# Kernel tuning notes

Hardware: AMD Instinct MI355X
Metric: run time of the kernel (lower is better)

Reference implementation:

```python
import jax, jax.numpy as jnp
import numpy as np

NUM_EXPERTS = 8
TOP_K = 2
AUX_COEF = 0.01
B, S, D, H = 4, 2048, 1024, 684


def setup_inputs() -> dict:
    key = jax.random.key(0)
    ks = jax.random.split(key, 5)
    scale_d = 1.0 / np.sqrt(D)
    scale_h = 1.0 / np.sqrt(H)
    return {
        "x": jax.random.normal(ks[0], (B, S, D), dtype=jnp.float32),
        "router_w": jax.random.normal(ks[1], (NUM_EXPERTS, D), dtype=jnp.float32) * scale_d,
        "w1": jax.random.normal(ks[2], (NUM_EXPERTS, H, D), dtype=jnp.float32) * scale_d,
        "w2": jax.random.normal(ks[3], (NUM_EXPERTS, D, H), dtype=jnp.float32) * scale_h,
        "w3": jax.random.normal(ks[4], (NUM_EXPERTS, H, D), dtype=jnp.float32) * scale_d,
    }


def reference(x, router_w, w1, w2, w3):
    b, s, d = x.shape
    xf = x.reshape(-1, d)                                   # [T, d]
    probs = jax.nn.softmax(xf @ router_w.T, axis=-1)        # [T, E]
    topk_probs, topk_idx = jax.lax.top_k(probs, TOP_K)      # [T, k]

    # aux load-balancing loss (uses top-1 assignment density)
    density = jnp.mean(jax.nn.one_hot(topk_idx[:, 0], NUM_EXPERTS, dtype=xf.dtype), axis=0)
    aux_loss = AUX_COEF * jnp.sum(density * probs.mean(axis=0)) * NUM_EXPERTS

    # per-token per-expert combine weight (sums probs if an expert repeats across slots)
    combine = jnp.sum(jax.nn.one_hot(topk_idx, NUM_EXPERTS, dtype=xf.dtype)
                      * topk_probs[..., None], axis=1)      # [T, E]

    out = jnp.zeros_like(xf)
    for e in range(NUM_EXPERTS):  # fixed small expert loop
        h = jax.nn.silu(xf @ w1[e].T) * (xf @ w3[e].T)      # [T, H] SwiGLU
        out = out + combine[:, e:e + 1] * (h @ w2[e].T)     # weighted scatter-combine
    return out.reshape(b, s, d), aux_loss
```

## Files before the change

kernel.cpp:

```cpp
#include <hip/hip_runtime.h>
#include <hip/hip_bf16.h>

#define T_TOK 8192
#define DMODEL 1024
#define HDIM 684
#define HPAD 704
#define NEXP 8

typedef short  bf16x8  __attribute__((ext_vector_type(8)));
typedef float  f32x4   __attribute__((ext_vector_type(4)));

__device__ inline unsigned short f2bu(float f) {
    __hip_bfloat16 h = __float2bfloat16(f);
    return *reinterpret_cast<unsigned short*>(&h);
}

typedef const __attribute__((address_space(1))) unsigned int* gas_p;
typedef __attribute__((address_space(3))) unsigned int* las_p;
__device__ inline void ld_lds16(const unsigned short* g, unsigned short* l) {
    __builtin_amdgcn_global_load_lds((gas_p)g, (las_p)l, 16, 0, 0);
}


__global__ __launch_bounds__(256) void cvt_w13(
    const float* __restrict__ w1, const float* __restrict__ w3,
    unsigned short* __restrict__ w1b, unsigned short* __restrict__ w3b, int n4)
{
    int i = blockIdx.x * 256 + threadIdx.x;
    const float* src; unsigned short* dst; int j;
    if (i < n4) { src = w1; dst = w1b; j = i; }
    else if (i < 2 * n4) { src = w3; dst = w3b; j = i - n4; }
    else return;
    float4 v = ((const float4*)src)[j];
    ushort4 o = make_ushort4(f2bu(v.x), f2bu(v.y), f2bu(v.z), f2bu(v.w));
    ((ushort4*)dst)[j] = o;
}

__global__ __launch_bounds__(256) void cvt_w2_pad(
    const float* __restrict__ w2, unsigned short* __restrict__ w2b, int n)
{
    int i = blockIdx.x * 256 + threadIdx.x;
    if (i >= n) return;
    int row = i / 176;
    int col = (i - row * 176) * 4;
    ushort4 o = make_ushort4(0, 0, 0, 0);
    if (col < HDIM) {
        float4 v = *(const float4*)(w2 + (size_t)row * HDIM + col);
        o = make_ushort4(f2bu(v.x), f2bu(v.y), f2bu(v.z), f2bu(v.w));
    }
    *(ushort4*)(w2b + (size_t)row * HPAD + col) = o;
}

__global__ __launch_bounds__(256) void moe_router(
    const float* __restrict__ x, const float* __restrict__ rw,
    unsigned short* __restrict__ xb,
    float* __restrict__ blk_psum, int* __restrict__ blk_t1, int* __restrict__ blk_pc,
    int* __restrict__ topk_idx, float* __restrict__ topk_p)
{
    __shared__ float sp[4][NEXP];
    __shared__ int   si1[4], si2[4];

    int lane = threadIdx.x & 63;
    int w    = threadIdx.x >> 6;
    int t    = blockIdx.x * 4 + w;
    const float* xr = x + (size_t)t * DMODEL;
    unsigned short* xbr = xb + (size_t)t * DMODEL;

    float acc[NEXP];
#pragma unroll
    for (int e = 0; e < NEXP; ++e) acc[e] = 0.f;
#pragma unroll
    for (int j = 0; j < DMODEL / 64; ++j) {
        float xv = xr[j * 64 + lane];
        xbr[j * 64 + lane] = f2bu(xv);
#pragma unroll
        for (int e = 0; e < NEXP; ++e)
            acc[e] += xv * rw[e * DMODEL + j * 64 + lane];
    }
#pragma unroll
    for (int off = 32; off > 0; off >>= 1) {
#pragma unroll
        for (int e = 0; e < NEXP; ++e)
            acc[e] += __shfl_xor(acc[e], off, 64);
    }
    if (lane == 0) {
        float m = acc[0];
#pragma unroll
        for (int e = 1; e < NEXP; ++e) m = fmaxf(m, acc[e]);
        float p[NEXP]; float s = 0.f;
#pragma unroll
        for (int e = 0; e < NEXP; ++e) { p[e] = expf(acc[e] - m); s += p[e]; }
        float inv = 1.f / s;
#pragma unroll
        for (int e = 0; e < NEXP; ++e) p[e] *= inv;
        int i1 = 0;
#pragma unroll
        for (int e = 1; e < NEXP; ++e) if (p[e] > p[i1]) i1 = e;
        int i2 = (i1 == 0) ? 1 : 0;
#pragma unroll
        for (int e = 0; e < NEXP; ++e) if (e != i1 && p[e] > p[i2]) i2 = e;

        topk_idx[t * 2 + 0] = i1;  topk_idx[t * 2 + 1] = i2;
        topk_p[t * 2 + 0] = p[i1]; topk_p[t * 2 + 1] = p[i2];
#pragma unroll
        for (int e = 0; e < NEXP; ++e) sp[w][e] = p[e];
        si1[w] = i1; si2[w] = i2;
    }
    __syncthreads();
    if (threadIdx.x < NEXP) {
        int e = threadIdx.x;
        float ps = sp[0][e] + sp[1][e] + sp[2][e] + sp[3][e];
        int t1 = (si1[0] == e) + (si1[1] == e) + (si1[2] == e) + (si1[3] == e);
        int pc = t1 + (si2[0] == e) + (si2[1] == e) + (si2[2] == e) + (si2[3] == e);
        blk_psum[blockIdx.x * NEXP + e] = ps;
        blk_t1[blockIdx.x * NEXP + e]  = t1;
        blk_pc[blockIdx.x * NEXP + e]  = pc;
    }
}

__global__ __launch_bounds__(256) void moe_scan(
    const float* __restrict__ blk_psum, const int* __restrict__ blk_t1,
    const int* __restrict__ blk_pc,
    int* pair_count, int* offsets, int* cursor, float* aux_out)
{
    __shared__ float rp[256][NEXP];
    __shared__ int   rt[256][NEXP], rc[256][NEXP];
    __shared__ float tp[NEXP];
    __shared__ int   tt1[NEXP], tpc[NEXP];

    int tid = threadIdx.x;
    float lp[NEXP]; int lt[NEXP], lc[NEXP];
#pragma unroll
    for (int e = 0; e < NEXP; ++e) { lp[e] = 0.f; lt[e] = 0; lc[e] = 0; }
    for (int b = tid; b < 2048; b += 256)
#pragma unroll
        for (int e = 0; e < NEXP; ++e) {
            lp[e] += blk_psum[b * NEXP + e];
            lt[e] += blk_t1[b * NEXP + e];
            lc[e] += blk_pc[b * NEXP + e];
        }
#pragma unroll
    for (int e = 0; e < NEXP; ++e) { rp[tid][e] = lp[e]; rt[tid][e] = lt[e]; rc[tid][e] = lc[e]; }
    __syncthreads();
    if (tid < NEXP) {
        float s = 0.f; int t1 = 0, pc = 0;
        for (int i = 0; i < 256; ++i) { s += rp[i][tid]; t1 += rt[i][tid]; pc += rc[i][tid]; }
        tp[tid] = s; tt1[tid] = t1; tpc[tid] = pc;
        pair_count[tid] = pc;
    }
    __syncthreads();
    if (tid == 0) {
        int run = 0;
        for (int e = 0; e < NEXP; ++e) { offsets[e] = run; cursor[e] = run; run += tpc[e]; }
        float s = 0.f;
        for (int e = 0; e < NEXP; ++e)
            s += ((float)tt1[e] / (float)T_TOK) * (tp[e] / (float)T_TOK);
        aux_out[0] = 0.01f * s * (float)NEXP;
    }
}

__global__ __launch_bounds__(256) void moe_scatter(
    const int* __restrict__ topk_idx, const float* __restrict__ topk_p,
    int* cursor, int* __restrict__ pair_token, float* __restrict__ pair_prob)
{
    __shared__ int lcnt[NEXP], gbase[NEXP];
    int tid = threadIdx.x;
    if (tid < NEXP) lcnt[tid] = 0;
    __syncthreads();
    int t = blockIdx.x * 256 + tid;
    int e0 = topk_idx[t * 2 + 0], e1 = topk_idx[t * 2 + 1];
    int p0 = atomicAdd(&lcnt[e0], 1);
    int p1 = atomicAdd(&lcnt[e1], 1);
    __syncthreads();
    if (tid < NEXP) gbase[tid] = atomicAdd(&cursor[tid], lcnt[tid]);
    __syncthreads();
    int q0 = gbase[e0] + p0, q1 = gbase[e1] + p1;
    pair_token[q0] = t; pair_prob[q0] = topk_p[t * 2 + 0];
    pair_token[q1] = t; pair_prob[q1] = topk_p[t * 2 + 1];
}


__global__ __launch_bounds__(512) void moe_ffn1(
    const unsigned short* __restrict__ xb, const unsigned short* __restrict__ w1b,
    const unsigned short* __restrict__ w3b,
    const int* __restrict__ pair_count, const int* __restrict__ offsets,
    const int* __restrict__ pair_token,
    unsigned short* __restrict__ h)
{
    int e   = blockIdx.z;
    int cnt = pair_count[e];
    int m0  = blockIdx.y * 128;
    if (m0 >= cnt) return;
    int base = offsets[e];
    int n0   = blockIdx.x * 128;

    __shared__ unsigned short aT[2][4096];
    __shared__ unsigned short b1T[2][4096];
    __shared__ unsigned short b3T[2][4096];

    int tid  = threadIdx.x;
    int lane = tid & 63, wave = tid >> 6;
    int wm = wave >> 1, wn = wave & 1;

    int srow = lane >> 2;
    int ksg  = (lane & 3) ^ ((lane >> 3) & 3);
    int arow = m0 + wave * 16 + srow; if (arow >= cnt) arow = cnt - 1;
    const unsigned short* ap  = xb + (size_t)pair_token[base + arow] * DMODEL + ksg * 8;
    int brow = n0 + wave * 16 + srow; if (brow > HDIM - 1) brow = HDIM - 1;
    const unsigned short* b1p = w1b + ((size_t)e * HDIM + brow) * DMODEL + ksg * 8;
    const unsigned short* b3p = w3b + ((size_t)e * HDIM + brow) * DMODEL + ksg * 8;
    unsigned short* lA[2]  = { &aT[0][wave * 512],  &aT[1][wave * 512]  };
    unsigned short* lB1[2] = { &b1T[0][wave * 512], &b1T[1][wave * 512] };
    unsigned short* lB3[2] = { &b3T[0][wave * 512], &b3T[1][wave * 512] };

    f32x4 acc1[2][4], acc3[2][4];
#pragma unroll
    for (int i = 0; i < 2; ++i)
#pragma unroll
        for (int j = 0; j < 4; ++j) { acc1[i][j] = (f32x4)(0.f); acc3[i][j] = (f32x4)(0.f); }

    int fr  = lane & 15;
    int sz8 = ((lane >> 4) ^ ((fr >> 1) & 3)) * 8;

    ld_lds16(ap, lA[0]);
    ld_lds16(b1p, lB1[0]);
    ld_lds16(b3p, lB3[0]);

    const int NIT = DMODEL / 32;
    for (int it = 0; it < NIT; ++it) {
        int buf = it & 1;
        __syncthreads();
        if (it + 1 < NIT) {
            int nk = (it + 1) * 32;
            ld_lds16(ap + nk,  lA[buf ^ 1]);
            ld_lds16(b1p + nk, lB1[buf ^ 1]);
            ld_lds16(b3p + nk, lB3[buf ^ 1]);
        }
        const unsigned short* cA  = aT[buf];
        const unsigned short* cB1 = b1T[buf];
        const unsigned short* cB3 = b3T[buf];

        bf16x8 aF[2];
#pragma unroll
        for (int i = 0; i < 2; ++i)
            aF[i] = *(const bf16x8*)&cA[(wm * 32 + i * 16 + fr) * 32 + sz8];
#pragma unroll
        for (int j = 0; j < 4; ++j) {
            int row = (wn * 64 + j * 16 + fr) * 32 + sz8;
            bf16x8 b1F = *(const bf16x8*)&cB1[row];
            bf16x8 b3F = *(const bf16x8*)&cB3[row];
#pragma unroll
            for (int i = 0; i < 2; ++i) {
                acc1[i][j] = __builtin_amdgcn_mfma_f32_16x16x32_bf16(aF[i], b1F, acc1[i][j], 0, 0, 0);
                acc3[i][j] = __builtin_amdgcn_mfma_f32_16x16x32_bf16(aF[i], b3F, acc3[i][j], 0, 0, 0);
            }
        }
    }

    int cbase = n0 + wn * 64 + fr;
    int rbase = m0 + wm * 32 + (lane >> 4) * 4;
#pragma unroll
    for (int i = 0; i < 2; ++i) {
#pragma unroll
        for (int r = 0; r < 4; ++r) {
            int gr = rbase + i * 16 + r;
            if (gr >= cnt) continue;
            unsigned short* hrow = h + (size_t)(base + gr) * HPAD;
#pragma unroll
            for (int j = 0; j < 4; ++j) {
                int col = cbase + j * 16;
                if (col >= HPAD) continue;
                float v1 = acc1[i][j][r];
                float hv = (col < HDIM) ? (v1 / (1.f + expf(-v1))) * acc3[i][j][r] : 0.f;
                hrow[col] = f2bu(hv);
            }
        }
    }
}

__global__ __launch_bounds__(512) void moe_ffn2(
    const unsigned short* __restrict__ h, const unsigned short* __restrict__ w2b,
    const int* __restrict__ pair_count, const int* __restrict__ offsets,
    const int* __restrict__ pair_token, const float* __restrict__ pair_prob,
    float* __restrict__ out)
{
    int e   = blockIdx.z;
    int cnt = pair_count[e];
    int m0  = blockIdx.y * 128;
    if (m0 >= cnt) return;
    int base = offsets[e];
    int n0   = blockIdx.x * 128;

    __shared__ unsigned short aT[2][4096];
    __shared__ unsigned short bT[2][4096];

    int tid  = threadIdx.x;
    int lane = tid & 63, wave = tid >> 6;
    int wm = wave >> 1, wn = wave & 1;

    int srow = lane >> 2;
    int ksg  = (lane & 3) ^ ((lane >> 3) & 3);
    int arow = m0 + wave * 16 + srow; if (arow >= cnt) arow = cnt - 1;
    const unsigned short* ap = h + (size_t)(base + arow) * HPAD + ksg * 8;
    const unsigned short* bp = w2b + ((size_t)e * DMODEL + n0 + wave * 16 + srow) * HPAD + ksg * 8;
    unsigned short* lA[2] = { &aT[0][wave * 512], &aT[1][wave * 512] };
    unsigned short* lB[2] = { &bT[0][wave * 512], &bT[1][wave * 512] };

    f32x4 acc[2][4];
#pragma unroll
    for (int i = 0; i < 2; ++i)
#pragma unroll
        for (int j = 0; j < 4; ++j) acc[i][j] = (f32x4)(0.f);

    int fr  = lane & 15;
    int sz8 = ((lane >> 4) ^ ((fr >> 1) & 3)) * 8;

    ld_lds16(ap, lA[0]);
    ld_lds16(bp, lB[0]);

    const int NIT = HPAD / 32;
    for (int it = 0; it < NIT; ++it) {
        int buf = it & 1;
        __syncthreads();
        if (it + 1 < NIT) {
            int nk = (it + 1) * 32;
            ld_lds16(ap + nk, lA[buf ^ 1]);
            ld_lds16(bp + nk, lB[buf ^ 1]);
        }
        const unsigned short* cA = aT[buf];
        const unsigned short* cB = bT[buf];

        bf16x8 aF[2];
#pragma unroll
        for (int i = 0; i < 2; ++i)
            aF[i] = *(const bf16x8*)&cA[(wm * 32 + i * 16 + fr) * 32 + sz8];
#pragma unroll
        for (int j = 0; j < 4; ++j) {
            bf16x8 bF = *(const bf16x8*)&cB[(wn * 64 + j * 16 + fr) * 32 + sz8];
#pragma unroll
            for (int i = 0; i < 2; ++i)
                acc[i][j] = __builtin_amdgcn_mfma_f32_16x16x32_bf16(aF[i], bF, acc[i][j], 0, 0, 0);
        }
    }

    int cbase = n0 + wn * 64 + fr;
    int rbase = m0 + wm * 32 + (lane >> 4) * 4;
#pragma unroll
    for (int i = 0; i < 2; ++i) {
#pragma unroll
        for (int r = 0; r < 4; ++r) {
            int gr = rbase + i * 16 + r;
            if (gr >= cnt) continue;
            int gp = base + gr;
            float pw = pair_prob[gp];
            float* orow = out + (size_t)pair_token[gp] * DMODEL;
#pragma unroll
            for (int j = 0; j < 4; ++j)
                atomicAdd(&orow[cbase + j * 16], pw * acc[i][j][r]);
        }
    }
}

extern "C" void kernel_launch(void* const* d_in, const int* in_sizes, int n_in,
                              void* d_out, int out_size, void* d_ws, size_t ws_size,
                              hipStream_t stream)
{
    const float* x  = (const float*)d_in[0];
    const float* rw = (const float*)d_in[1];
    const float* w1 = (const float*)d_in[2];
    const float* w2 = (const float*)d_in[3];
    const float* w3 = (const float*)d_in[4];
    float* out = (float*)d_out;

    char* ws = (char*)d_ws;
    int*   pair_count = (int*)(ws + 0);
    int*   offsets    = (int*)(ws + 32);
    int*   cursor     = (int*)(ws + 64);
    float* blk_psum   = (float*)(ws + 256);
    int*   blk_t1     = (int*)(ws + 65792);
    int*   blk_pc     = (int*)(ws + 131328);
    int*   topk_idx   = (int*)(ws + 196864);
    float* topk_p     = (float*)(ws + 262400);
    int*   pair_token = (int*)(ws + 327936);
    float* pair_prob  = (float*)(ws + 393472);
    unsigned short* xb  = (unsigned short*)(ws + 459264);
    unsigned short* w1b = (unsigned short*)(ws + 17236480);
    unsigned short* w3b = (unsigned short*)(ws + 28443136);
    unsigned short* w2b = (unsigned short*)(ws + 39649792);
    unsigned short* hbuf= (unsigned short*)(ws + 51184128);

    hipMemsetAsync(d_out, 0, (size_t)out_size * sizeof(float), stream);

    int n4 = NEXP * HDIM * DMODEL / 4;
    cvt_w13<<<(2 * n4 + 255) / 256, 256, 0, stream>>>(w1, w3, w1b, w3b, n4);
    cvt_w2_pad<<<(NEXP * DMODEL * (HPAD / 4) + 255) / 256, 256, 0, stream>>>(w2, w2b, NEXP * DMODEL * (HPAD / 4));

    moe_router <<<T_TOK / 4, 256, 0, stream>>>(x, rw, xb, blk_psum, blk_t1, blk_pc, topk_idx, topk_p);
    moe_scan   <<<1, 256, 0, stream>>>(blk_psum, blk_t1, blk_pc, pair_count, offsets, cursor,
                                       out + (size_t)T_TOK * DMODEL);
    moe_scatter<<<T_TOK / 256, 256, 0, stream>>>(topk_idx, topk_p, cursor, pair_token, pair_prob);

    moe_ffn1<<<dim3(6, 64, 8), 512, 0, stream>>>(xb, w1b, w3b, pair_count, offsets, pair_token, hbuf);
    moe_ffn2<<<dim3(8, 64, 8), 512, 0, stream>>>(hbuf, w2b, pair_count, offsets, pair_token, pair_prob, out);
}
```

Measured before the change: 326.7 us.

## Triple-buffer FFN GEMMs, widen ffn2 tile, fuse weight casts, shuffle-reduce scan

Both FFN GEMM kernels move from double to triple-buffered LDS, with explicit vmcnt waits and raw barriers so global-to-LDS loads run two stages ahead. They also raise MFMA wave priority and add an occupancy hint to launch_bounds. ffn2 widens its N tile to 256, which halves the grid and the A-tile reloads. The two weight conversion kernels are merged into one launch, and the scan kernel's reduction now uses wave shuffles instead of a large LDS array. The hand-written vmcnt counts depend on how many loads are in flight per thread, so they risk being wrong, and the larger LDS footprint may lower occupancy.

```diff
diff --git a/kernel.cpp b/kernel.cpp
--- a/kernel.cpp
+++ b/kernel.cpp
@@ -22,27 +22,24 @@
 }
 
 
-__global__ __launch_bounds__(256) void cvt_w13(
-    const float* __restrict__ w1, const float* __restrict__ w3,
-    unsigned short* __restrict__ w1b, unsigned short* __restrict__ w3b, int n4)
+__global__ __launch_bounds__(256) void cvt_all(
+    const float* __restrict__ w1, const float* __restrict__ w3, const float* __restrict__ w2,
+    unsigned short* __restrict__ w1b, unsigned short* __restrict__ w3b,
+    unsigned short* __restrict__ w2b, int n4, int n2)
 {
     int i = blockIdx.x * 256 + threadIdx.x;
-    const float* src; unsigned short* dst; int j;
-    if (i < n4) { src = w1; dst = w1b; j = i; }
-    else if (i < 2 * n4) { src = w3; dst = w3b; j = i - n4; }
-    else return;
-    float4 v = ((const float4*)src)[j];
-    ushort4 o = make_ushort4(f2bu(v.x), f2bu(v.y), f2bu(v.z), f2bu(v.w));
-    ((ushort4*)dst)[j] = o;
-}
-
-__global__ __launch_bounds__(256) void cvt_w2_pad(
-    const float* __restrict__ w2, unsigned short* __restrict__ w2b, int n)
-{
-    int i = blockIdx.x * 256 + threadIdx.x;
-    if (i >= n) return;
-    int row = i / 176;
-    int col = (i - row * 176) * 4;
+    if (i < 2 * n4) {
+        const float* src; unsigned short* dst; int j;
+        if (i < n4) { src = w1; dst = w1b; j = i; }
+        else        { src = w3; dst = w3b; j = i - n4; }
+        float4 v = ((const float4*)src)[j];
+        ((ushort4*)dst)[j] = make_ushort4(f2bu(v.x), f2bu(v.y), f2bu(v.z), f2bu(v.w));
+        return;
+    }
+    int j = i - 2 * n4;
+    if (j >= n2) return;
+    int row = j / 176;
+    int col = (j - row * 176) * 4;
     ushort4 o = make_ushort4(0, 0, 0, 0);
     if (col < HDIM) {
         float4 v = *(const float4*)(w2 + (size_t)row * HDIM + col);
@@ -123,12 +120,13 @@
     const int* __restrict__ blk_pc,
     int* pair_count, int* offsets, int* cursor, float* aux_out)
 {
-    __shared__ float rp[256][NEXP];
-    __shared__ int   rt[256][NEXP], rc[256][NEXP];
+    __shared__ float wp[4][NEXP];
+    __shared__ int   wt[4][NEXP], wc[4][NEXP];
     __shared__ float tp[NEXP];
     __shared__ int   tt1[NEXP], tpc[NEXP];
 
     int tid = threadIdx.x;
+    int lane = tid & 63, w = tid >> 6;
     float lp[NEXP]; int lt[NEXP], lc[NEXP];
 #pragma unroll
     for (int e = 0; e < NEXP; ++e) { lp[e] = 0.f; lt[e] = 0; lc[e] = 0; }
@@ -140,13 +138,26 @@
             lc[e] += blk_pc[b * NEXP + e];
         }
 #pragma unroll
-    for (int e = 0; e < NEXP; ++e) { rp[tid][e] = lp[e]; rt[tid][e] = lt[e]; rc[tid][e] = lc[e]; }
+    for (int off = 32; off > 0; off >>= 1) {
+#pragma unroll
+        for (int e = 0; e < NEXP; ++e) {
+            lp[e] += __shfl_xor(lp[e], off, 64);
+            lt[e] += __shfl_xor(lt[e], off, 64);
+            lc[e] += __shfl_xor(lc[e], off, 64);
+        }
+    }
+    if (lane == 0) {
+#pragma unroll
+        for (int e = 0; e < NEXP; ++e) { wp[w][e] = lp[e]; wt[w][e] = lt[e]; wc[w][e] = lc[e]; }
+    }
     __syncthreads();
     if (tid < NEXP) {
-        float s = 0.f; int t1 = 0, pc = 0;
-        for (int i = 0; i < 256; ++i) { s += rp[i][tid]; t1 += rt[i][tid]; pc += rc[i][tid]; }
-        tp[tid] = s; tt1[tid] = t1; tpc[tid] = pc;
-        pair_count[tid] = pc;
+        int e = tid;
+        float s = wp[0][e] + wp[1][e] + wp[2][e] + wp[3][e];
+        int t1 = wt[0][e] + wt[1][e] + wt[2][e] + wt[3][e];
+        int pc = wc[0][e] + wc[1][e] + wc[2][e] + wc[3][e];
+        tp[e] = s; tt1[e] = t1; tpc[e] = pc;
+        pair_count[e] = pc;
     }
     __syncthreads();
     if (tid == 0) {
@@ -180,7 +191,7 @@
 }
 
 
-__global__ __launch_bounds__(512) void moe_ffn1(
+__global__ __launch_bounds__(512, 4) void moe_ffn1(
     const unsigned short* __restrict__ xb, const unsigned short* __restrict__ w1b,
     const unsigned short* __restrict__ w3b,
     const int* __restrict__ pair_count, const int* __restrict__ offsets,
@@ -194,9 +205,9 @@
     int base = offsets[e];
     int n0   = blockIdx.x * 128;
 
-    __shared__ unsigned short aT[2][4096];
-    __shared__ unsigned short b1T[2][4096];
-    __shared__ unsigned short b3T[2][4096];
+    __shared__ unsigned short aT[3 * 4096];
+    __shared__ unsigned short b1T[3 * 4096];
+    __shared__ unsigned short b3T[3 * 4096];
 
     int tid  = threadIdx.x;
     int lane = tid & 63, wave = tid >> 6;
@@ -209,9 +220,9 @@
     int brow = n0 + wave * 16 + srow; if (brow > HDIM - 1) brow = HDIM - 1;
     const unsigned short* b1p = w1b + ((size_t)e * HDIM + brow) * DMODEL + ksg * 8;
     const unsigned short* b3p = w3b + ((size_t)e * HDIM + brow) * DMODEL + ksg * 8;
-    unsigned short* lA[2]  = { &aT[0][wave * 512],  &aT[1][wave * 512]  };
-    unsigned short* lB1[2] = { &b1T[0][wave * 512], &b1T[1][wave * 512] };
-    unsigned short* lB3[2] = { &b3T[0][wave * 512], &b3T[1][wave * 512] };
+    unsigned short* sA  = aT  + wave * 512;
+    unsigned short* sB1 = b1T + wave * 512;
+    unsigned short* sB3 = b3T + wave * 512;
 
     f32x4 acc1[2][4], acc3[2][4];
 #pragma unroll
@@ -222,28 +233,36 @@
     int fr  = lane & 15;
     int sz8 = ((lane >> 4) ^ ((fr >> 1) & 3)) * 8;
 
-    ld_lds16(ap, lA[0]);
-    ld_lds16(b1p, lB1[0]);
-    ld_lds16(b3p, lB3[0]);
+    ld_lds16(ap,        sA);
+    ld_lds16(b1p,       sB1);
+    ld_lds16(b3p,       sB3);
+    ld_lds16(ap  + 32,  sA  + 4096);
+    ld_lds16(b1p + 32,  sB1 + 4096);
+    ld_lds16(b3p + 32,  sB3 + 4096);
 
     const int NIT = DMODEL / 32;
     for (int it = 0; it < NIT; ++it) {
-        int buf = it & 1;
-        __syncthreads();
-        if (it + 1 < NIT) {
-            int nk = (it + 1) * 32;
-            ld_lds16(ap + nk,  lA[buf ^ 1]);
-            ld_lds16(b1p + nk, lB1[buf ^ 1]);
-            ld_lds16(b3p + nk, lB3[buf ^ 1]);
-        }
-        const unsigned short* cA  = aT[buf];
-        const unsigned short* cB1 = b1T[buf];
-        const unsigned short* cB3 = b3T[buf];
+        int buf = it % 3;
+        if (it + 1 < NIT) asm volatile("s_waitcnt vmcnt(3)" ::: "memory");
+        else              asm volatile("s_waitcnt vmcnt(0)" ::: "memory");
+        __builtin_amdgcn_s_barrier();
+        asm volatile("" ::: "memory");
+        if (it + 2 < NIT) {
+            int nb = (it + 2) % 3;
+            int nk = (it + 2) * 32;
+            ld_lds16(ap  + nk, sA  + nb * 4096);
+            ld_lds16(b1p + nk, sB1 + nb * 4096);
+            ld_lds16(b3p + nk, sB3 + nb * 4096);
+        }
+        const unsigned short* cA  = aT  + buf * 4096;
+        const unsigned short* cB1 = b1T + buf * 4096;
+        const unsigned short* cB3 = b3T + buf * 4096;
 
         bf16x8 aF[2];
 #pragma unroll
         for (int i = 0; i < 2; ++i)
             aF[i] = *(const bf16x8*)&cA[(wm * 32 + i * 16 + fr) * 32 + sz8];
+        __builtin_amdgcn_s_setprio(1);
 #pragma unroll
         for (int j = 0; j < 4; ++j) {
             int row = (wn * 64 + j * 16 + fr) * 32 + sz8;
@@ -255,6 +274,7 @@
                 acc3[i][j] = __builtin_amdgcn_mfma_f32_16x16x32_bf16(aF[i], b3F, acc3[i][j], 0, 0, 0);
             }
         }
+        __builtin_amdgcn_s_setprio(0);
     }
 
     int cbase = n0 + wn * 64 + fr;
@@ -278,7 +298,7 @@
     }
 }
 
-__global__ __launch_bounds__(512) void moe_ffn2(
+__global__ __launch_bounds__(512, 4) void moe_ffn2(
     const unsigned short* __restrict__ h, const unsigned short* __restrict__ w2b,
     const int* __restrict__ pair_count, const int* __restrict__ offsets,
     const int* __restrict__ pair_token, const float* __restrict__ pair_prob,
@@ -289,10 +309,10 @@
     int m0  = blockIdx.y * 128;
     if (m0 >= cnt) return;
     int base = offsets[e];
-    int n0   = blockIdx.x * 128;
-
-    __shared__ unsigned short aT[2][4096];
-    __shared__ unsigned short bT[2][4096];
+    int n0   = blockIdx.x * 256;
+
+    __shared__ unsigned short aT[3 * 4096];
+    __shared__ unsigned short bT[3 * 8192];
 
     int tid  = threadIdx.x;
     int lane = tid & 63, wave = tid >> 6;
@@ -302,48 +322,59 @@
     int ksg  = (lane & 3) ^ ((lane >> 3) & 3);
     int arow = m0 + wave * 16 + srow; if (arow >= cnt) arow = cnt - 1;
     const unsigned short* ap = h + (size_t)(base + arow) * HPAD + ksg * 8;
-    const unsigned short* bp = w2b + ((size_t)e * DMODEL + n0 + wave * 16 + srow) * HPAD + ksg * 8;
-    unsigned short* lA[2] = { &aT[0][wave * 512], &aT[1][wave * 512] };
-    unsigned short* lB[2] = { &bT[0][wave * 512], &bT[1][wave * 512] };
-
-    f32x4 acc[2][4];
+    const unsigned short* bp = w2b + ((size_t)e * DMODEL + n0 + wave * 32 + srow) * HPAD + ksg * 8;
+    unsigned short* sA = aT + wave * 512;
+    unsigned short* sB = bT + wave * 1024;
+
+    f32x4 acc[2][8];
 #pragma unroll
     for (int i = 0; i < 2; ++i)
 #pragma unroll
-        for (int j = 0; j < 4; ++j) acc[i][j] = (f32x4)(0.f);
+        for (int j = 0; j < 8; ++j) acc[i][j] = (f32x4)(0.f);
 
     int fr  = lane & 15;
     int sz8 = ((lane >> 4) ^ ((fr >> 1) & 3)) * 8;
 
-    ld_lds16(ap, lA[0]);
-    ld_lds16(bp, lB[0]);
+    ld_lds16(ap,                  sA);
+    ld_lds16(bp,                  sB);
+    ld_lds16(bp + 16 * HPAD,      sB + 512);
+    ld_lds16(ap + 32,             sA + 4096);
+    ld_lds16(bp + 32,             sB + 8192);
+    ld_lds16(bp + 16 * HPAD + 32, sB + 8192 + 512);
 
     const int NIT = HPAD / 32;
     for (int it = 0; it < NIT; ++it) {
-        int buf = it & 1;
-        __syncthreads();
-        if (it + 1 < NIT) {
-            int nk = (it + 1) * 32;
-            ld_lds16(ap + nk, lA[buf ^ 1]);
-            ld_lds16(bp + nk, lB[buf ^ 1]);
-        }
-        const unsigned short* cA = aT[buf];
-        const unsigned short* cB = bT[buf];
+        int buf = it % 3;
+        if (it + 1 < NIT) asm volatile("s_waitcnt vmcnt(3)" ::: "memory");
+        else              asm volatile("s_waitcnt vmcnt(0)" ::: "memory");
+        __builtin_amdgcn_s_barrier();
+        asm volatile("" ::: "memory");
+        if (it + 2 < NIT) {
+            int nb = (it + 2) % 3;
+            int nk = (it + 2) * 32;
+            ld_lds16(ap + nk,             sA + nb * 4096);
+            ld_lds16(bp + nk,             sB + nb * 8192);
+            ld_lds16(bp + 16 * HPAD + nk, sB + nb * 8192 + 512);
+        }
+        const unsigned short* cA = aT + buf * 4096;
+        const unsigned short* cB = bT + buf * 8192;
 
         bf16x8 aF[2];
 #pragma unroll
         for (int i = 0; i < 2; ++i)
             aF[i] = *(const bf16x8*)&cA[(wm * 32 + i * 16 + fr) * 32 + sz8];
-#pragma unroll
-        for (int j = 0; j < 4; ++j) {
-            bf16x8 bF = *(const bf16x8*)&cB[(wn * 64 + j * 16 + fr) * 32 + sz8];
+        __builtin_amdgcn_s_setprio(1);
+#pragma unroll
+        for (int j = 0; j < 8; ++j) {
+            bf16x8 bF = *(const bf16x8*)&cB[(wn * 128 + j * 16 + fr) * 32 + sz8];
 #pragma unroll
             for (int i = 0; i < 2; ++i)
                 acc[i][j] = __builtin_amdgcn_mfma_f32_16x16x32_bf16(aF[i], bF, acc[i][j], 0, 0, 0);
         }
-    }
-
-    int cbase = n0 + wn * 64 + fr;
+        __builtin_amdgcn_s_setprio(0);
+    }
+
+    int cbase = n0 + wn * 128 + fr;
     int rbase = m0 + wm * 32 + (lane >> 4) * 4;
 #pragma unroll
     for (int i = 0; i < 2; ++i) {
@@ -355,7 +386,7 @@
             float pw = pair_prob[gp];
             float* orow = out + (size_t)pair_token[gp] * DMODEL;
 #pragma unroll
-            for (int j = 0; j < 4; ++j)
+            for (int j = 0; j < 8; ++j)
                 atomicAdd(&orow[cbase + j * 16], pw * acc[i][j][r]);
         }
     }
@@ -392,8 +423,8 @@
     hipMemsetAsync(d_out, 0, (size_t)out_size * sizeof(float), stream);
 
     int n4 = NEXP * HDIM * DMODEL / 4;
-    cvt_w13<<<(2 * n4 + 255) / 256, 256, 0, stream>>>(w1, w3, w1b, w3b, n4);
-    cvt_w2_pad<<<(NEXP * DMODEL * (HPAD / 4) + 255) / 256, 256, 0, stream>>>(w2, w2b, NEXP * DMODEL * (HPAD / 4));
+    int n2 = NEXP * DMODEL * (HPAD / 4);
+    cvt_all<<<(2 * n4 + n2 + 255) / 256, 256, 0, stream>>>(w1, w3, w2, w1b, w3b, w2b, n4, n2);
 
     moe_router <<<T_TOK / 4, 256, 0, stream>>>(x, rw, xb, blk_psum, blk_t1, blk_pc, topk_idx, topk_p);
     moe_scan   <<<1, 256, 0, stream>>>(blk_psum, blk_t1, blk_pc, pair_count, offsets, cursor,
@@ -401,5 +432,5 @@
     moe_scatter<<<T_TOK / 256, 256, 0, stream>>>(topk_idx, topk_p, cursor, pair_token, pair_prob);
 
     moe_ffn1<<<dim3(6, 64, 8), 512, 0, stream>>>(xb, w1b, w3b, pair_count, offsets, pair_token, hbuf);
-    moe_ffn2<<<dim3(8, 64, 8), 512, 0, stream>>>(hbuf, w2b, pair_count, offsets, pair_token, pair_prob, out);
-}
+    moe_ffn2<<<dim3(4, 64, 8), 512, 0, stream>>>(hbuf, w2b, pair_count, offsets, pair_token, pair_prob, out);
+}
```

Result: no change. 326.3 us (-0.1%).
